# Performance work log

Measured on AMD Instinct MI355X. Metric: run time of the kernel, lower is better.

Reference implementation:

```python
import jax, jax.numpy as jnp
import numpy as np

NUM_HEADS = 16

def _rmsnorm(x, w):
    eps = jnp.finfo(x.dtype).eps  # torch nn.RMSNorm default eps
    ms = jnp.mean(x * x, axis=-1, keepdims=True)
    return x * jax.lax.rsqrt(ms + eps) * w

def _heads(x):
    B, S, D = x.shape
    return x.reshape(B, S, NUM_HEADS, D // NUM_HEADS)

def _attn(q, k, v):
    # q:[B,Sq,H,D] k,v:[B,Sk,H,D]; non-causal softmax attention
    scale = 1.0 / np.sqrt(q.shape[-1]).astype(np.float32)
    s = jnp.einsum('bqhd,bkhd->bhqk', q, k) * scale
    p = jax.nn.softmax(s, axis=-1)
    return jnp.einsum('bhqk,bkhd->bqhd', p, v)

def _gate(ctx, W1, b1, W2, b2):
    # Linear -> SiLU -> Linear(dim->1) -> sigmoid ; returns [B,S,1]
    h = jax.nn.silu(ctx @ W1.T + b1)
    return jax.nn.sigmoid(h @ W2.T + b2)

def setup_inputs() -> dict:
    key = jax.random.key(0)
    ks = jax.random.split(key, 20)
    B, Sq, Sk, St, dim = 4, 512, 2048, 512, 1024
    n = lambda k, shp, s=1.0: jax.random.normal(k, shp, jnp.float32) * s
    W = lambda k, o, i: n(k, (o, i), 0.02)
    return {
        'queries': n(ks[0], (B, Sq, dim)),
        'context_visual': n(ks[1], (B, Sk, dim)),
        'context_text': n(ks[2], (B, St, dim)),
        'w_norm_q': jnp.ones((dim,), jnp.float32),
        'w_norm_v': jnp.ones((dim,), jnp.float32),
        'w_norm_t': jnp.ones((dim,), jnp.float32),
        'Wq': W(ks[3], dim, dim), 'bq': n(ks[4], (dim,), 0.02),
        'Wk_vis': W(ks[5], dim, dim), 'bk_vis': jnp.zeros((dim,), jnp.float32),
        'Wv_vis': W(ks[6], dim, dim), 'bv_vis': jnp.zeros((dim,), jnp.float32),
        'Wk_text': W(ks[7], dim, dim), 'bk_text': jnp.zeros((dim,), jnp.float32),
        'Wv_text': W(ks[8], dim, dim), 'bv_text': jnp.zeros((dim,), jnp.float32),
        'Wg1v': W(ks[9], dim, dim), 'bg1v': jnp.zeros((dim,), jnp.float32),
        'Wg2v': W(ks[10], 1, dim), 'bg2v': jnp.zeros((1,), jnp.float32),
        'Wg1t': W(ks[11], dim, dim), 'bg1t': jnp.zeros((dim,), jnp.float32),
        'Wg2t': W(ks[12], 1, dim), 'bg2t': jnp.zeros((1,), jnp.float32),
        'Wo': W(ks[13], dim, dim), 'bo': jnp.zeros((dim,), jnp.float32),
    }

def reference(queries, context_visual, context_text,
              w_norm_q, w_norm_v, w_norm_t,
              Wq, bq, Wk_vis, bk_vis, Wv_vis, bv_vis,
              Wk_text, bk_text, Wv_text, bv_text,
              Wg1v, bg1v, Wg2v, bg2v, Wg1t, bg1t, Wg2t, bg2t,
              Wo, bo):
    residual = queries
    qn = _rmsnorm(queries, w_norm_q)
    cv = _rmsnorm(context_visual, w_norm_v)
    ct = _rmsnorm(context_text, w_norm_t)
    q = _heads(qn @ Wq.T + bq)
    k_vis = _heads(cv @ Wk_vis.T + bk_vis)
    v_vis = _heads(cv @ Wv_vis.T + bv_vis)
    v_vis = v_vis * _gate(cv, Wg1v, bg1v, Wg2v, bg2v)[..., None]  # [B,Sk,1,1]
    h = _attn(q, k_vis, v_vis)
    k_text = _heads(ct @ Wk_text.T + bk_text)
    v_text = _heads(ct @ Wv_text.T + bv_text)
    v_text = v_text * _gate(ct, Wg1t, bg1t, Wg2t, bg2t)[..., None]
    h = h + _attn(q, k_text, v_text)
    B, Sq, H, D = h.shape
    out = h.reshape(B, Sq, H * D) @ Wo.T + bo  # dropout p=0 -> identity
    return residual + out
```

## Files before the change

kernel.cpp:

```cpp
#include <hip/hip_runtime.h>
#include <hip/hip_bf16.h>

typedef __attribute__((ext_vector_type(4))) float f32x4;
typedef __attribute__((ext_vector_type(8))) short s16x8;
typedef __attribute__((ext_vector_type(4))) short s16x4;
using bf16 = __hip_bfloat16;

static constexpr int BB  = 4;
static constexpr int SQ  = 512;
static constexpr int SKV = 2048;
static constexpr int SKT = 512;
static constexpr int DIM = 1024;
static constexpr int NH  = 16;
static constexpr int HD  = 64;

#define MFMA32(A,B,C) __builtin_amdgcn_mfma_f32_16x16x32_bf16(A,B,C,0,0,0)

#if __has_builtin(__builtin_amdgcn_mfma_f32_16x16x16_bf16)
  #define MFMA16(A,B,C) __builtin_amdgcn_mfma_f32_16x16x16_bf16(A,B,C,0,0,0)
#elif __has_builtin(__builtin_amdgcn_mfma_f32_16x16x16bf16_1k)
  #define MFMA16(A,B,C) __builtin_amdgcn_mfma_f32_16x16x16bf16_1k(A,B,C,0,0,0)
#else
  #define MFMA16(A,B,C) (C)
#endif

#define SBAR() asm volatile("s_barrier" ::: "memory")

__device__ __forceinline__ float b2f(short s) {
  unsigned int u = ((unsigned int)(unsigned short)s) << 16;
  float f; __builtin_memcpy(&f, &u, 4); return f;
}
__device__ __forceinline__ short f2s(float f) {
  bf16 h = __float2bfloat16(f); short s; __builtin_memcpy(&s, &h, 2); return s;
}

__device__ __forceinline__ void gload16(const void* g, void* l) {
  __builtin_amdgcn_global_load_lds(
      (const __attribute__((address_space(1))) void*)g,
      (__attribute__((address_space(3))) void*)l, 16, 0, 0);
}

static constexpr float QSCALE = 0.180336880111120426f;

struct PrepArgs {
  const float* csrc[10]; bf16* cdst[10]; int cn[10];
  const float* nx[3]; const float* nw[3]; bf16* ny[3];
};
__global__ __launch_bounds__(256) void prep_kernel(PrepArgs a) {
  const int bx = blockIdx.x;
  if (bx < 10240) {
    const int y = bx >> 10;
    const int i = ((bx & 1023) * 256 + threadIdx.x) * 4;
    if (i >= a.cn[y]) return;
    const float4 v = *(const float4*)(a.csrc[y] + i);
    bf16* d = a.cdst[y] + i;
    d[0] = __float2bfloat16(v.x); d[1] = __float2bfloat16(v.y);
    d[2] = __float2bfloat16(v.z); d[3] = __float2bfloat16(v.w);
    return;
  }
  const int j = bx - 10240;
  int t, row;
  if (j < 2048) { t = 0; row = j; }
  else if (j < 10240) { t = 1; row = j - 2048; }
  else { t = 2; row = j - 10240; }
  const float* x = a.nx[t] + (size_t)row * DIM;
  const float4 v = *(const float4*)(x + threadIdx.x * 4);
  float ss = v.x*v.x + v.y*v.y + v.z*v.z + v.w*v.w;
  #pragma unroll
  for (int m = 32; m >= 1; m >>= 1) ss += __shfl_xor(ss, m);
  __shared__ float red[4];
  if ((threadIdx.x & 63) == 0) red[threadIdx.x >> 6] = ss;
  __syncthreads();
  ss = red[0] + red[1] + red[2] + red[3];
  const float sc = rsqrtf(ss * (1.0f / DIM) + 1.1920928955078125e-07f);
  const float4 w = *(const float4*)(a.nw[t] + threadIdx.x * 4);
  bf16* y = a.ny[t] + (size_t)row * DIM + threadIdx.x * 4;
  y[0] = __float2bfloat16(v.x * sc * w.x);
  y[1] = __float2bfloat16(v.y * sc * w.y);
  y[2] = __float2bfloat16(v.z * sc * w.z);
  y[3] = __float2bfloat16(v.w * sc * w.w);
}

struct PSlot { const bf16* A; const bf16* W; const float* bias;
               bf16* Cb; int epi; int sksh; };
struct PArgs { PSlot s[7]; };

__global__ __launch_bounds__(512, 2) void proj256(PArgs a) {
  __shared__ char lds[131072];
  const int tid = threadIdx.x, lane = tid & 63, wave = tid >> 6;
  const int m16 = lane & 15, g16 = lane >> 4;
  const int wm = wave >> 2, wn = wave & 3;

  const int i = (blockIdx.x & 7) * 64 + (blockIdx.x >> 3);
  int slot, rem;
  if (i < 384) { slot = i >> 7; rem = i & 127; }
  else { const int j = i - 384; slot = 3 + (j >> 5); rem = j & 31; }
  const PSlot S = a.s[slot];
  const int bn = rem & 3, bm = rem >> 2;

  const bf16* Ab = S.A + (size_t)bm * 256 * DIM;
  const bf16* Wb = S.W + (size_t)bn * 256 * DIM;

  auto stageAh = [&](int k0, int buf, int h) {
    #pragma unroll
    for (int q = 0; q < 2; ++q) {
      const int idx = (h * 2 + q) * 512 + tid;
      const int row = idx >> 3, g = (idx & 7) ^ (row & 7);
      gload16(Ab + (size_t)row * DIM + k0 + g * 8,
              &lds[buf * 65536 + (h * 2 + q) * 8192 + wave * 1024]);
    }
  };
  auto stageBfull = [&](int k0, int buf) {
    #pragma unroll
    for (int q = 0; q < 4; ++q) {
      const int idx = q * 512 + tid;
      const int row = idx >> 3, g = (idx & 7) ^ (row & 7);
      gload16(Wb + (size_t)row * DIM + k0 + g * 8,
              &lds[buf * 65536 + 32768 + q * 8192 + wave * 1024]);
    }
  };

  f32x4 acc[8][4];
  #pragma unroll
  for (int x = 0; x < 8; ++x)
    #pragma unroll
    for (int y = 0; y < 4; ++y)
      #pragma unroll
      for (int r = 0; r < 4; ++r) acc[x][y][r] = 0.0f;

  stageAh(0, 0, 0); stageAh(0, 0, 1);
  stageBfull(0, 0);
  stageBfull(64, 1);
  asm volatile("s_waitcnt vmcnt(4)" ::: "memory");
  SBAR();

  constexpr int NT = DIM / 64;
  for (int t = 0; t < NT; ++t) {
    const int buf = t & 1;
    const char* A0 = &lds[buf * 65536];
    const char* B0 = A0 + 32768;
    s16x8 af[4], bfk[4];

    #pragma unroll
    for (int mi = 0; mi < 4; ++mi) {
      const int row = wm * 128 + mi * 16 + m16;
      af[mi] = *(const s16x8*)(A0 + row * 128 + ((g16 ^ (m16 & 7)) * 16));
    }
    #pragma unroll
    for (int ni = 0; ni < 4; ++ni) {
      const int row = wn * 64 + ni * 16 + m16;
      bfk[ni] = *(const s16x8*)(B0 + row * 128 + ((g16 ^ (m16 & 7)) * 16));
    }
    if (t + 1 < NT) stageAh((t + 1) * 64, buf ^ 1, 0);
    SBAR();
    __builtin_amdgcn_s_setprio(1);
    #pragma unroll
    for (int mi = 0; mi < 4; ++mi)
      #pragma unroll
      for (int ni = 0; ni < 4; ++ni)
        acc[mi][ni] = MFMA32(af[mi], bfk[ni], acc[mi][ni]);
    __builtin_amdgcn_s_setprio(0);
    SBAR();

    #pragma unroll
    for (int mi = 0; mi < 4; ++mi) {
      const int row = wm * 128 + 64 + mi * 16 + m16;
      af[mi] = *(const s16x8*)(A0 + row * 128 + ((g16 ^ (m16 & 7)) * 16));
    }
    if (t + 1 < NT) stageAh((t + 1) * 64, buf ^ 1, 1);
    SBAR();
    __builtin_amdgcn_s_setprio(1);
    #pragma unroll
    for (int mi = 0; mi < 4; ++mi)
      #pragma unroll
      for (int ni = 0; ni < 4; ++ni)
        acc[4 + mi][ni] = MFMA32(af[mi], bfk[ni], acc[4 + mi][ni]);
    __builtin_amdgcn_s_setprio(0);
    SBAR();

    #pragma unroll
    for (int mi = 0; mi < 4; ++mi) {
      const int row = wm * 128 + mi * 16 + m16;
      af[mi] = *(const s16x8*)(A0 + row * 128 + (((4 + g16) ^ (m16 & 7)) * 16));
    }
    #pragma unroll
    for (int ni = 0; ni < 4; ++ni) {
      const int row = wn * 64 + ni * 16 + m16;
      bfk[ni] = *(const s16x8*)(B0 + row * 128 + (((4 + g16) ^ (m16 & 7)) * 16));
    }
    SBAR();
    __builtin_amdgcn_s_setprio(1);
    #pragma unroll
    for (int mi = 0; mi < 4; ++mi)
      #pragma unroll
      for (int ni = 0; ni < 4; ++ni)
        acc[mi][ni] = MFMA32(af[mi], bfk[ni], acc[mi][ni]);
    __builtin_amdgcn_s_setprio(0);
    SBAR();

    #pragma unroll
    for (int mi = 0; mi < 4; ++mi) {
      const int row = wm * 128 + 64 + mi * 16 + m16;
      af[mi] = *(const s16x8*)(A0 + row * 128 + (((4 + g16) ^ (m16 & 7)) * 16));
    }
    if (t + 2 < NT) stageBfull((t + 2) * 64, buf);
    SBAR();
    __builtin_amdgcn_s_setprio(1);
    #pragma unroll
    for (int mi = 0; mi < 4; ++mi)
      #pragma unroll
      for (int ni = 0; ni < 4; ++ni)
        acc[4 + mi][ni] = MFMA32(af[mi], bfk[ni], acc[4 + mi][ni]);
    __builtin_amdgcn_s_setprio(0);
    if (t < NT - 2)       { asm volatile("s_waitcnt vmcnt(4)" ::: "memory"); }
    else if (t == NT - 2) { asm volatile("s_waitcnt vmcnt(0)" ::: "memory"); }
    SBAR();
  }

  const int r0 = bm * 256 + wm * 128, c0 = bn * 256 + wn * 64;
  if (S.epi >= 3) {
    const float sc = (S.epi == 3) ? QSCALE : 1.0f;
    const int msk = (1 << S.sksh) - 1;
    #pragma unroll
    for (int ng = 0; ng < 4; ++ng) {
      const int col = c0 + ng * 16 + m16;
      const int hh = col >> 6, d = col & 63;
      const float bv = S.bias[col];
      #pragma unroll
      for (int mg = 0; mg < 8; ++mg) {
        const int rowb = r0 + mg * 16 + g16 * 4;
        #pragma unroll
        for (int r = 0; r < 4; ++r) {
          const int m = rowb + r;
          const int bb2 = m >> S.sksh, tok = m & msk;
          S.Cb[(((size_t)(bb2 * NH + hh) << S.sksh) + tok) * HD + d] =
              __float2bfloat16((acc[mg][ng][r] + bv) * sc);
        }
      }
    }
  } else {
    #pragma unroll
    for (int ng = 0; ng < 4; ++ng) {
      const int col = c0 + ng * 16 + m16;
      const float bv = S.bias[col];
      #pragma unroll
      for (int mg = 0; mg < 8; ++mg) {
        const int rowb = r0 + mg * 16 + g16 * 4;
        #pragma unroll
        for (int r = 0; r < 4; ++r) {
          float v = acc[mg][ng][r] + bv;
          const size_t idx = (size_t)(rowb + r) * DIM + col;
          if (S.epi == 1) { v = v / (1.0f + __expf(-v)); S.Cb[idx] = __float2bfloat16(v); }
          else            { S.Cb[idx] = __float2bfloat16(v); }
        }
      }
    }
  }
}

struct GSlot { const bf16* A; const bf16* W; const float* bias;
               const float* resid; float* Cf; };
__global__ __launch_bounds__(256) void gemm_out(GSlot S) {
  constexpr int K = DIM;
  __shared__ alignas(16) char sA[4096];
  __shared__ alignas(16) char sB[8192];
  const int tid = threadIdx.x, lane = tid & 63, wave = tid >> 6;
  const int bm = blockIdx.x, bn = blockIdx.y;
  const int m16 = lane & 15, g16 = lane >> 4;

  f32x4 acc[4][2];
  #pragma unroll
  for (int i = 0; i < 4; ++i)
    #pragma unroll
    for (int j = 0; j < 2; ++j)
      #pragma unroll
      for (int r = 0; r < 4; ++r) acc[i][j][r] = 0.0f;

  const bf16* Ab = S.A + (size_t)bm * 64 * K;
  const bf16* Wb = S.W + (size_t)bn * 128 * K;

  for (int t = 0; t < K / 32; ++t) {
    const int k0 = t * 32;
    {
      const int row = tid >> 2, sg = (tid & 3) ^ (row & 3);
      gload16(Ab + (size_t)row * K + k0 + sg * 8, &sA[wave * 1024]);
    }
    #pragma unroll
    for (int p = 0; p < 2; ++p) {
      const int idx = p * 256 + tid;
      const int row = idx >> 2, sg = (idx & 3) ^ (row & 3);
      gload16(Wb + (size_t)row * K + k0 + sg * 8, &sB[p * 4096 + wave * 1024]);
    }
    __syncthreads();
    s16x8 af[4], bfr[2];
    #pragma unroll
    for (int mi = 0; mi < 4; ++mi) {
      const int row = mi * 16 + m16;
      af[mi] = *(const s16x8*)(&sA[row * 64 + (g16 ^ (m16 & 3)) * 16]);
    }
    #pragma unroll
    for (int ni = 0; ni < 2; ++ni) {
      const int row = wave * 32 + ni * 16 + m16;
      bfr[ni] = *(const s16x8*)(&sB[row * 64 + (g16 ^ (m16 & 3)) * 16]);
    }
    #pragma unroll
    for (int mi = 0; mi < 4; ++mi)
      #pragma unroll
      for (int ni = 0; ni < 2; ++ni)
        acc[mi][ni] = MFMA32(af[mi], bfr[ni], acc[mi][ni]);
    __syncthreads();
  }

  const int r0 = bm * 64, c0 = bn * 128 + wave * 32;
  #pragma unroll
  for (int ni = 0; ni < 2; ++ni) {
    const int col = c0 + ni * 16 + m16;
    const float bv = S.bias[col];
    #pragma unroll
    for (int mi = 0; mi < 4; ++mi) {
      const int rowb = r0 + mi * 16 + g16 * 4;
      #pragma unroll
      for (int r = 0; r < 4; ++r) {
        const size_t idx = (size_t)(rowb + r) * DIM + col;
        S.Cf[idx] = acc[mi][ni][r] + bv + S.resid[idx];
      }
    }
  }
}

__global__ __launch_bounds__(256) void gate2_kernel(
    const bf16* __restrict__ g1v, const bf16* __restrict__ w2v,
    const float* __restrict__ b2v, float* __restrict__ gv,
    const bf16* __restrict__ g1t, const bf16* __restrict__ w2t,
    const float* __restrict__ b2t, float* __restrict__ gt)
{
  const int lane = threadIdx.x & 63, wave = threadIdx.x >> 6;
  int row = blockIdx.x * 4 + wave;
  const bf16* x; const bf16* w2; const float* b2; float* gate;
  if (row < BB * SKV) { x = g1v + (size_t)row * DIM; w2 = w2v; b2 = b2v; gate = gv + row; }
  else { row -= BB * SKV; x = g1t + (size_t)row * DIM; w2 = w2t; b2 = b2t; gate = gt + row; }
  float sum = 0.0f;
  #pragma unroll
  for (int c = 0; c < 2; ++c) {
    const int i0 = c * 512 + lane * 8;
    const s16x8 xv = *(const s16x8*)(x + i0);
    const s16x8 wv = *(const s16x8*)(w2 + i0);
    #pragma unroll
    for (int j = 0; j < 8; ++j) sum += b2f(xv[j]) * b2f(wv[j]);
  }
  #pragma unroll
  for (int m = 32; m >= 1; m >>= 1) sum += __shfl_xor(sum, m);
  if (lane == 0) *gate = 1.0f / (1.0f + __expf(-(sum + b2[0])));
}

__global__ __launch_bounds__(256) void vtrans2_kernel(
    const bf16* __restrict__ Vv, const float* __restrict__ gv, bf16* __restrict__ VTv,
    const bf16* __restrict__ Vt, const float* __restrict__ gt, bf16* __restrict__ VTt)
{
  __shared__ alignas(16) short tile[64][72];
  int kt = blockIdx.x;
  const bf16* V; const float* gate; bf16* VT; int Sk;
  if (kt < SKV / 64) { V = Vv; gate = gv; VT = VTv; Sk = SKV; }
  else { kt -= SKV / 64; V = Vt; gate = gt; VT = VTt; Sk = SKT; }
  const int h = blockIdx.y, b = blockIdx.z;
  const int tid = threadIdx.x;
  #pragma unroll
  for (int i = 0; i < 2; ++i) {
    const int c = tid + i * 256;
    const int kr = c >> 3, d0 = (c & 7) * 8;
    const float g = gate[(size_t)b * Sk + kt * 64 + kr];
    const s16x8 v = *(const s16x8*)(V + ((size_t)(b*Sk + kt*64 + kr)*NH + h)*HD + d0);
    #pragma unroll
    for (int j = 0; j < 8; ++j) tile[kr][d0 + j] = f2s(b2f(v[j]) * g);
  }
  __syncthreads();
  #pragma unroll
  for (int i = 0; i < 2; ++i) {
    const int c = tid + i * 256;
    const int d = c >> 3, k0 = (c & 7) * 8;
    s16x8 v;
    #pragma unroll
    for (int j = 0; j < 8; ++j) v[j] = tile[k0 + j][d];
    *(s16x8*)(VT + ((size_t)(b*NH + h)*HD + d)*Sk + kt*64 + k0) = v;
  }
}

__global__ __launch_bounds__(512, 2) void attn_kernel(
    const bf16* __restrict__ Qh,
    const bf16* __restrict__ K1h, const bf16* __restrict__ VT1,
    const bf16* __restrict__ K2h, const bf16* __restrict__ VT2,
    bf16* __restrict__ Hout)
{
  __shared__ alignas(16) char sK[2][2][8192];
  __shared__ alignas(16) char sVT[2][2][8192];
  const int tid = threadIdx.x, lane = tid & 63, wave = tid >> 6;
  const int hb = blockIdx.x;
  const int h = hb & 15, b = hb >> 4;
  const int wq = wave & 3, hf = wave >> 2;
  const int q0 = blockIdx.y * 64 + wq * 16;
  const int m16 = lane & 15, g16 = lane >> 4;

  const bf16* qrow = Qh + ((size_t)(b*NH + h)*SQ + q0 + m16)*HD;
  const s16x8 qf0 = *(const s16x8*)(qrow + g16 * 8);
  const s16x8 qf1 = *(const s16x8*)(qrow + 32 + g16 * 8);

  const bf16* K1b  = K1h + (size_t)(b*NH + h) * SKV * HD;
  const bf16* K2b  = K2h + (size_t)(b*NH + h) * SKT * HD;
  const bf16* VT1b = VT1 + (size_t)(b*NH + h) * HD * SKV;
  const bf16* VT2b = VT2 + (size_t)(b*NH + h) * HD * SKT;

  constexpr int NC1 = SKV / 128, NC = NC1 + SKT / 128;

  auto stage = [&](int c, int buf) {
    const int ctx = (c >= NC1);
    const bf16* Kb  = ctx ? K2b  : K1b;
    const bf16* VTb = ctx ? VT2b : VT1b;
    const int Sk = ctx ? SKT : SKV;
    const int cc = ctx ? c - NC1 : c;
    const int b0 = cc * 64, b1 = (Sk >> 1) + cc * 64;
    const int r = tid >> 3, g = (tid & 7) ^ (r & 7);
    gload16(Kb  + (size_t)(b0 + r) * HD + g * 8, &sK[buf][0][wave * 1024]);
    gload16(Kb  + (size_t)(b1 + r) * HD + g * 8, &sK[buf][1][wave * 1024]);
    gload16(VTb + (size_t)r * Sk + b0 + g * 8,   &sVT[buf][0][wave * 1024]);
    gload16(VTb + (size_t)r * Sk + b1 + g * 8,   &sVT[buf][1][wave * 1024]);
  };

  f32x4 o[4], ov[4];
  float mx, l, mxv, lv;
  #pragma unroll
  for (int i = 0; i < 4; ++i)
    #pragma unroll
    for (int r = 0; r < 4; ++r) { o[i][r] = 0.0f; ov[i][r] = 0.0f; }
  mx = -1e30f; l = 0.0f; mxv = -1e30f; lv = 0.0f;

  auto chunk = [&](int buf) {
    const char* kbase = &sK[buf][hf][0];
    const char* vbase = &sVT[buf][hf][0];
    f32x4 s[4];
    #pragma unroll
    for (int nt = 0; nt < 4; ++nt) {
      const char* kr = kbase + (nt * 16 + m16) * 128;
      const s16x8 kf0 = *(const s16x8*)(kr + ((g16    ) ^ (m16 & 7)) * 16);
      const s16x8 kf1 = *(const s16x8*)(kr + ((4 + g16) ^ (m16 & 7)) * 16);
      f32x4 a2; a2[0] = 0; a2[1] = 0; a2[2] = 0; a2[3] = 0;
      a2 = MFMA32(kf0, qf0, a2);
      a2 = MFMA32(kf1, qf1, a2);
      s[nt] = a2;
    }
    float mc = s[0][0];
    #pragma unroll
    for (int nt = 0; nt < 4; ++nt)
      #pragma unroll
      for (int r = 0; r < 4; ++r) mc = fmaxf(mc, s[nt][r]);
    mc = fmaxf(mc, __shfl_xor(mc, 16));
    mc = fmaxf(mc, __shfl_xor(mc, 32));
    const float mnew = fmaxf(mx, mc);
    const float alpha = exp2f(mx - mnew);
    mx = mnew;
    float p[4][4]; float rs = 0.0f;
    #pragma unroll
    for (int nt = 0; nt < 4; ++nt)
      #pragma unroll
      for (int r = 0; r < 4; ++r) { p[nt][r] = exp2f(s[nt][r] - mnew); rs += p[nt][r]; }
    rs += __shfl_xor(rs, 16);
    rs += __shfl_xor(rs, 32);
    l = l * alpha + rs;
    float av[4];
    #pragma unroll
    for (int r = 0; r < 4; ++r) av[r] = __shfl(alpha, g16 * 4 + r);
    #pragma unroll
    for (int nd = 0; nd < 4; ++nd)
      #pragma unroll
      for (int r = 0; r < 4; ++r) o[nd][r] *= av[r];
    #pragma unroll
    for (int nt = 0; nt < 4; ++nt) {
      s16x4 pa;
      pa[0] = f2s(p[nt][0]); pa[1] = f2s(p[nt][1]);
      pa[2] = f2s(p[nt][2]); pa[3] = f2s(p[nt][3]);
      #pragma unroll
      for (int nd = 0; nd < 4; ++nd) {
        const int d = nd * 16 + m16;
        const int g = (nt * 2 + (g16 >> 1)) ^ (m16 & 7);
        const s16x4 vf = *(const s16x4*)(vbase + d * 128 + g * 16 + (g16 & 1) * 8);
        o[nd] = MFMA16(pa, vf, o[nd]);
      }
    }
  };

  stage(0, 0);
  asm volatile("s_waitcnt vmcnt(0)" ::: "memory");
  SBAR();

  int buf = 0;
  for (int c = 0; c < NC; ++c) {
    if (c + 1 < NC) stage(c + 1, buf ^ 1);
    chunk(buf);
    if (c == NC1 - 1) {
      #pragma unroll
      for (int nd = 0; nd < 4; ++nd) ov[nd] = o[nd];
      mxv = mx; lv = l;
      #pragma unroll
      for (int nd = 0; nd < 4; ++nd)
        #pragma unroll
        for (int r = 0; r < 4; ++r) o[nd][r] = 0.0f;
      mx = -1e30f; l = 0.0f;
    }
    asm volatile("s_waitcnt vmcnt(0)" ::: "memory");
    SBAR();
    buf ^= 1;
  }

  float* mo = (float*)&sK[0][0][0];
  float* ml = (float*)&sVT[0][0][0];
  if (hf) {
    #pragma unroll
    for (int nd = 0; nd < 4; ++nd)
      #pragma unroll
      for (int r = 0; r < 4; ++r) {
        const int rl = wq * 16 + g16 * 4 + r;
        mo[rl * 64 + nd * 16 + m16]        = ov[nd][r];
        mo[4096 + rl * 64 + nd * 16 + m16] = o[nd][r];
      }
    if (g16 == 0) {
      ml[(wq * 4 + 0) * 16 + m16] = mxv; ml[(wq * 4 + 1) * 16 + m16] = lv;
      ml[(wq * 4 + 2) * 16 + m16] = mx;  ml[(wq * 4 + 3) * 16 + m16] = l;
    }
  }
  __syncthreads();
  if (!hf) {
    float of[4][4];
    #pragma unroll
    for (int ctx = 0; ctx < 2; ++ctx) {
      const float mb = ml[(wq * 4 + ctx * 2 + 0) * 16 + m16];
      const float lb = ml[(wq * 4 + ctx * 2 + 1) * 16 + m16];
      const float ma = ctx ? mx : mxv;
      const float la = ctx ? l  : lv;
      const float ms = fmaxf(ma, mb);
      const float aA = exp2f(ma - ms), aB = exp2f(mb - ms);
      const float lt = la * aA + lb * aB;
      float aAv[4], aBv[4], ltv[4];
      #pragma unroll
      for (int r = 0; r < 4; ++r) {
        aAv[r] = __shfl(aA, g16 * 4 + r);
        aBv[r] = __shfl(aB, g16 * 4 + r);
        ltv[r] = __shfl(lt, g16 * 4 + r);
      }
      #pragma unroll
      for (int nd = 0; nd < 4; ++nd)
        #pragma unroll
        for (int r = 0; r < 4; ++r) {
          const int rl = wq * 16 + g16 * 4 + r;
          const float ob = mo[ctx * 4096 + rl * 64 + nd * 16 + m16];
          const float oa = ctx ? o[nd][r] : ov[nd][r];
          const float res = (oa * aAv[r] + ob * aBv[r]) / ltv[r];
          if (ctx == 0) of[nd][r] = res; else of[nd][r] += res;
        }
    }
    #pragma unroll
    for (int nd = 0; nd < 4; ++nd)
      #pragma unroll
      for (int r = 0; r < 4; ++r) {
        const int row = q0 + g16 * 4 + r;
        Hout[((size_t)(b*SQ + row)*NH + h)*HD + nd*16 + m16] =
            __float2bfloat16(of[nd][r]);
      }
  }
}

extern "C" void kernel_launch(void* const* d_in, const int* in_sizes, int n_in,
                              void* d_out, int out_size, void* d_ws, size_t ws_size,
                              hipStream_t stream)
{
  const float* queries = (const float*)d_in[0];
  const float* ctx_v   = (const float*)d_in[1];
  const float* ctx_t   = (const float*)d_in[2];
  const float* w_nq = (const float*)d_in[3];
  const float* w_nv = (const float*)d_in[4];
  const float* w_nt = (const float*)d_in[5];
  const float* Wq   = (const float*)d_in[6];  const float* bq   = (const float*)d_in[7];
  const float* Wk_v = (const float*)d_in[8];  const float* bk_v = (const float*)d_in[9];
  const float* Wv_v = (const float*)d_in[10]; const float* bv_v = (const float*)d_in[11];
  const float* Wk_t = (const float*)d_in[12]; const float* bk_t = (const float*)d_in[13];
  const float* Wv_t = (const float*)d_in[14]; const float* bv_t = (const float*)d_in[15];
  const float* Wg1v = (const float*)d_in[16]; const float* bg1v = (const float*)d_in[17];
  const float* Wg2v = (const float*)d_in[18]; const float* bg2v = (const float*)d_in[19];
  const float* Wg1t = (const float*)d_in[20]; const float* bg1t = (const float*)d_in[21];
  const float* Wg2t = (const float*)d_in[22]; const float* bg2t = (const float*)d_in[23];
  const float* Wo   = (const float*)d_in[24]; const float* bo   = (const float*)d_in[25];

  char* ws = (char*)d_ws;
  size_t off = 0;
  auto alloc = [&](size_t n) { void* p = ws + off; off += (n + 255) & ~(size_t)255; return p; };

  const size_t MATB = (size_t)DIM * DIM * 2;
  bf16* WqB   = (bf16*)alloc(MATB);
  bf16* WkvB  = (bf16*)alloc(MATB);
  bf16* WvvB  = (bf16*)alloc(MATB);
  bf16* WktB  = (bf16*)alloc(MATB);
  bf16* WvtB  = (bf16*)alloc(MATB);
  bf16* Wg1vB = (bf16*)alloc(MATB);
  bf16* Wg1tB = (bf16*)alloc(MATB);
  bf16* WoB   = (bf16*)alloc(MATB);
  bf16* Wg2vB = (bf16*)alloc(2048);
  bf16* Wg2tB = (bf16*)alloc(2048);

  bf16* qn  = (bf16*)alloc((size_t)BB*SQ*DIM*2);
  bf16* cv  = (bf16*)alloc((size_t)BB*SKV*DIM*2);
  bf16* ct  = (bf16*)alloc((size_t)BB*SKT*DIM*2);
  bf16* qb  = (bf16*)alloc((size_t)BB*SQ*DIM*2);
  bf16* kvB = (bf16*)alloc((size_t)BB*SKV*DIM*2);
  bf16* ktB = (bf16*)alloc((size_t)BB*SKT*DIM*2);
  bf16* vtV = (bf16*)alloc((size_t)BB*SKV*DIM*2);
  bf16* vtT = (bf16*)alloc((size_t)BB*SKT*DIM*2);
  bf16* vScrV = (bf16*)alloc((size_t)BB*SKV*DIM*2);
  bf16* vScrT = (bf16*)alloc((size_t)BB*SKT*DIM*2);
  bf16* g1V   = (bf16*)alloc((size_t)BB*SKV*DIM*2);
  bf16* g1T   = (bf16*)alloc((size_t)BB*SKT*DIM*2);
  float* gateV = (float*)alloc((size_t)BB*SKV*4);
  float* gateT = (float*)alloc((size_t)BB*SKT*4);
  bf16* hB  = (bf16*)alloc((size_t)BB*SQ*DIM*2);
  (void)ws_size; (void)n_in; (void)in_sizes; (void)out_size;

  PrepArgs pr;
  const float* wsrc[10] = {Wq, Wk_v, Wv_v, Wk_t, Wv_t, Wg1v, Wg1t, Wo, Wg2v, Wg2t};
  bf16* wdst[10] = {WqB, WkvB, WvvB, WktB, WvtB, Wg1vB, Wg1tB, WoB, Wg2vB, Wg2tB};
  for (int i = 0; i < 10; ++i) {
    pr.csrc[i] = wsrc[i]; pr.cdst[i] = wdst[i];
    pr.cn[i] = (i < 8) ? DIM * DIM : DIM;
  }
  pr.nx[0] = queries; pr.nx[1] = ctx_v; pr.nx[2] = ctx_t;
  pr.nw[0] = w_nq;    pr.nw[1] = w_nv;  pr.nw[2] = w_nt;
  pr.ny[0] = qn;      pr.ny[1] = cv;    pr.ny[2] = ct;
  prep_kernel<<<dim3(10240 + 12288), 256, 0, stream>>>(pr);

  PArgs pa;
  pa.s[0] = {cv, WkvB,  bk_v, kvB,   4, 11};
  pa.s[1] = {cv, WvvB,  bv_v, vScrV, 0, 0};
  pa.s[2] = {cv, Wg1vB, bg1v, g1V,   1, 0};
  pa.s[3] = {qn, WqB,   bq,   qb,    3, 9};
  pa.s[4] = {ct, WktB,  bk_t, ktB,   4, 9};
  pa.s[5] = {ct, WvtB,  bv_t, vScrT, 0, 0};
  pa.s[6] = {ct, Wg1tB, bg1t, g1T,   1, 0};
  proj256<<<dim3(512), 512, 0, stream>>>(pa);

  gate2_kernel<<<dim3((BB*SKV + BB*SKT) / 4), 256, 0, stream>>>(
      g1V, Wg2vB, bg2v, gateV, g1T, Wg2tB, bg2t, gateT);
  vtrans2_kernel<<<dim3(SKV/64 + SKT/64, NH, BB), 256, 0, stream>>>(
      vScrV, gateV, vtV, vScrT, gateT, vtT);

  attn_kernel<<<dim3(NH*BB, SQ/64), 512, 0, stream>>>(qb, kvB, vtV, ktB, vtT, hB);

  GSlot go{hB, WoB, bo, queries, (float*)d_out};
  gemm_out<<<dim3(BB*SQ/64, 8), 256, 0, stream>>>(go);
}
```

Baseline: 195.8 us.

## Give each attention wave its own query rows and triple-buffer K/V chunks

The attention kernel stops splitting the key range across two wave halves. All 8 waves now handle distinct 16-row query tiles, 128 queries per block, and share each 64-key K/VT chunk. This removes the cross-wave LDS merge of partial softmax states and doubles reuse of each staged K/V tile. Loads move to a 3-stage ring with a prefetch distance of two. The grid is halved to 256 blocks, which may hurt occupancy across the CUs, and there are twice as many loop iterations per block.

```diff
diff --git a/kernel.cpp b/kernel.cpp
--- a/kernel.cpp
+++ b/kernel.cpp
@@ -391,13 +391,12 @@
     const bf16* __restrict__ K2h, const bf16* __restrict__ VT2,
     bf16* __restrict__ Hout)
 {
-  __shared__ alignas(16) char sK[2][2][8192];
-  __shared__ alignas(16) char sVT[2][2][8192];
+  __shared__ alignas(16) char sK[3][8192];
+  __shared__ alignas(16) char sVT[3][8192];
   const int tid = threadIdx.x, lane = tid & 63, wave = tid >> 6;
   const int hb = blockIdx.x;
   const int h = hb & 15, b = hb >> 4;
-  const int wq = wave & 3, hf = wave >> 2;
-  const int q0 = blockIdx.y * 64 + wq * 16;
+  const int q0 = blockIdx.y * 128 + wave * 16;
   const int m16 = lane & 15, g16 = lane >> 4;
 
   const bf16* qrow = Qh + ((size_t)(b*NH + h)*SQ + q0 + m16)*HD;
@@ -409,33 +408,49 @@
   const bf16* VT1b = VT1 + (size_t)(b*NH + h) * HD * SKV;
   const bf16* VT2b = VT2 + (size_t)(b*NH + h) * HD * SKT;
 
-  constexpr int NC1 = SKV / 128, NC = NC1 + SKT / 128;
+  constexpr int NCV = SKV / 64, NC = NCV + SKT / 64;
 
   auto stage = [&](int c, int buf) {
-    const int ctx = (c >= NC1);
+    const int ctx = (c >= NCV);
     const bf16* Kb  = ctx ? K2b  : K1b;
     const bf16* VTb = ctx ? VT2b : VT1b;
     const int Sk = ctx ? SKT : SKV;
-    const int cc = ctx ? c - NC1 : c;
-    const int b0 = cc * 64, b1 = (Sk >> 1) + cc * 64;
+    const int b0 = (ctx ? c - NCV : c) * 64;
     const int r = tid >> 3, g = (tid & 7) ^ (r & 7);
-    gload16(Kb  + (size_t)(b0 + r) * HD + g * 8, &sK[buf][0][wave * 1024]);
-    gload16(Kb  + (size_t)(b1 + r) * HD + g * 8, &sK[buf][1][wave * 1024]);
-    gload16(VTb + (size_t)r * Sk + b0 + g * 8,   &sVT[buf][0][wave * 1024]);
-    gload16(VTb + (size_t)r * Sk + b1 + g * 8,   &sVT[buf][1][wave * 1024]);
+    gload16(Kb  + (size_t)(b0 + r) * HD + g * 8, &sK[buf][wave * 1024]);
+    gload16(VTb + (size_t)r * Sk + b0 + g * 8,   &sVT[buf][wave * 1024]);
   };
 
-  f32x4 o[4], ov[4];
-  float mx, l, mxv, lv;
+  float of[4][4];
   #pragma unroll
   for (int i = 0; i < 4; ++i)
     #pragma unroll
-    for (int r = 0; r < 4; ++r) { o[i][r] = 0.0f; ov[i][r] = 0.0f; }
-  mx = -1e30f; l = 0.0f; mxv = -1e30f; lv = 0.0f;
+    for (int r = 0; r < 4; ++r) of[i][r] = 0.0f;
+
+  f32x4 o[4];
+  float mx = -1e30f, l = 0.0f;
+  #pragma unroll
+  for (int i = 0; i < 4; ++i)
+    #pragma unroll
+    for (int r = 0; r < 4; ++r) o[i][r] = 0.0f;
+
+  auto flush = [&]() {
+    float lb[4];
+    #pragma unroll
+    for (int r = 0; r < 4; ++r) lb[r] = __shfl(l, g16 * 4 + r);
+    #pragma unroll
+    for (int nd = 0; nd < 4; ++nd)
+      #pragma unroll
+      for (int r = 0; r < 4; ++r) {
+        of[nd][r] += o[nd][r] / lb[r];
+        o[nd][r] = 0.0f;
+      }
+    mx = -1e30f; l = 0.0f;
+  };
 
   auto chunk = [&](int buf) {
-    const char* kbase = &sK[buf][hf][0];
-    const char* vbase = &sVT[buf][hf][0];
+    const char* kbase = &sK[buf][0];
+    const char* vbase = &sVT[buf][0];
     f32x4 s[4];
     #pragma unroll
     for (int nt = 0; nt < 4; ++nt) {
@@ -488,83 +503,28 @@
   };
 
   stage(0, 0);
-  asm volatile("s_waitcnt vmcnt(0)" ::: "memory");
+  stage(1, 1);
+  asm volatile("s_waitcnt vmcnt(2)" ::: "memory");
   SBAR();
 
-  int buf = 0;
   for (int c = 0; c < NC; ++c) {
-    if (c + 1 < NC) stage(c + 1, buf ^ 1);
-    chunk(buf);
-    if (c == NC1 - 1) {
-      #pragma unroll
-      for (int nd = 0; nd < 4; ++nd) ov[nd] = o[nd];
-      mxv = mx; lv = l;
-      #pragma unroll
-      for (int nd = 0; nd < 4; ++nd)
-        #pragma unroll
-        for (int r = 0; r < 4; ++r) o[nd][r] = 0.0f;
-      mx = -1e30f; l = 0.0f;
-    }
-    asm volatile("s_waitcnt vmcnt(0)" ::: "memory");
-    SBAR();
-    buf ^= 1;
-  }
-
-  float* mo = (float*)&sK[0][0][0];
-  float* ml = (float*)&sVT[0][0][0];
-  if (hf) {
-    #pragma unroll
-    for (int nd = 0; nd < 4; ++nd)
-      #pragma unroll
-      for (int r = 0; r < 4; ++r) {
-        const int rl = wq * 16 + g16 * 4 + r;
-        mo[rl * 64 + nd * 16 + m16]        = ov[nd][r];
-        mo[4096 + rl * 64 + nd * 16 + m16] = o[nd][r];
-      }
-    if (g16 == 0) {
-      ml[(wq * 4 + 0) * 16 + m16] = mxv; ml[(wq * 4 + 1) * 16 + m16] = lv;
-      ml[(wq * 4 + 2) * 16 + m16] = mx;  ml[(wq * 4 + 3) * 16 + m16] = l;
-    }
-  }
-  __syncthreads();
-  if (!hf) {
-    float of[4][4];
-    #pragma unroll
-    for (int ctx = 0; ctx < 2; ++ctx) {
-      const float mb = ml[(wq * 4 + ctx * 2 + 0) * 16 + m16];
-      const float lb = ml[(wq * 4 + ctx * 2 + 1) * 16 + m16];
-      const float ma = ctx ? mx : mxv;
-      const float la = ctx ? l  : lv;
-      const float ms = fmaxf(ma, mb);
-      const float aA = exp2f(ma - ms), aB = exp2f(mb - ms);
-      const float lt = la * aA + lb * aB;
-      float aAv[4], aBv[4], ltv[4];
-      #pragma unroll
-      for (int r = 0; r < 4; ++r) {
-        aAv[r] = __shfl(aA, g16 * 4 + r);
-        aBv[r] = __shfl(aB, g16 * 4 + r);
-        ltv[r] = __shfl(lt, g16 * 4 + r);
-      }
-      #pragma unroll
-      for (int nd = 0; nd < 4; ++nd)
-        #pragma unroll
-        for (int r = 0; r < 4; ++r) {
-          const int rl = wq * 16 + g16 * 4 + r;
-          const float ob = mo[ctx * 4096 + rl * 64 + nd * 16 + m16];
-          const float oa = ctx ? o[nd][r] : ov[nd][r];
-          const float res = (oa * aAv[r] + ob * aBv[r]) / ltv[r];
-          if (ctx == 0) of[nd][r] = res; else of[nd][r] += res;
-        }
-    }
-    #pragma unroll
-    for (int nd = 0; nd < 4; ++nd)
-      #pragma unroll
-      for (int r = 0; r < 4; ++r) {
-        const int row = q0 + g16 * 4 + r;
-        Hout[((size_t)(b*SQ + row)*NH + h)*HD + nd*16 + m16] =
-            __float2bfloat16(of[nd][r]);
-      }
-  }
+    if (c + 2 < NC) stage(c + 2, (c + 2) % 3);
+    chunk(c % 3);
+    if (c == NCV - 1) flush();
+    if (c + 2 < NC) { asm volatile("s_waitcnt vmcnt(2)" ::: "memory"); }
+    else            { asm volatile("s_waitcnt vmcnt(0)" ::: "memory"); }
+    SBAR();
+  }
+  flush();
+
+  #pragma unroll
+  for (int nd = 0; nd < 4; ++nd)
+    #pragma unroll
+    for (int r = 0; r < 4; ++r) {
+      const int row = q0 + g16 * 4 + r;
+      Hout[((size_t)(b*SQ + row)*NH + h)*HD + nd*16 + m16] =
+          __float2bfloat16(of[nd][r]);
+    }
 }
 
 extern "C" void kernel_launch(void* const* d_in, const int* in_sizes, int n_in,
@@ -648,7 +608,7 @@
   vtrans2_kernel<<<dim3(SKV/64 + SKT/64, NH, BB), 256, 0, stream>>>(
       vScrV, gateV, vtV, vScrT, gateT, vtT);
 
-  attn_kernel<<<dim3(NH*BB, SQ/64), 512, 0, stream>>>(qb, kvB, vtV, ktB, vtT, hB);
+  attn_kernel<<<dim3(NH*BB, SQ/128), 512, 0, stream>>>(qb, kvB, vtV, ktB, vtT, hB);
 
   GSlot go{hB, WoB, bo, queries, (float*)d_out};
   gemm_out<<<dim3(BB*SQ/64, 8), 256, 0, stream>>>(go);
```

New measurement: 217.1 us. +10.9%, slower.

## Replace double-buffered projection GEMM pipeline with single-buffered load-wait-compute loop

Applied to the files above, without the earlier changes.

The projection GEMM kernel drops its two-stage LDS double buffer and interleaved prefetch schedule. It now loads each 64-wide K tile into a single 64KB buffer, waits for all loads, then runs the MFMAs. Launch bounds are raised to 4 blocks per CU to hide memory latency through occupancy instead of software pipelining. The cost is that global loads no longer overlap compute within a block, and 512 threads at 4 blocks per CU with 128 accumulator floats per thread may force register spills.

```diff
diff --git a/kernel.cpp b/kernel.cpp
--- a/kernel.cpp
+++ b/kernel.cpp
@@ -85,8 +85,8 @@
                bf16* Cb; int epi; int sksh; };
 struct PArgs { PSlot s[7]; };
 
-__global__ __launch_bounds__(512, 2) void proj256(PArgs a) {
-  __shared__ char lds[131072];
+__global__ __launch_bounds__(512, 4) void proj256(PArgs a) {
+  __shared__ char lds[65536];
   const int tid = threadIdx.x, lane = tid & 63, wave = tid >> 6;
   const int m16 = lane & 15, g16 = lane >> 4;
   const int wm = wave >> 2, wn = wave & 3;
@@ -101,22 +101,22 @@
   const bf16* Ab = S.A + (size_t)bm * 256 * DIM;
   const bf16* Wb = S.W + (size_t)bn * 256 * DIM;
 
-  auto stageAh = [&](int k0, int buf, int h) {
-    #pragma unroll
-    for (int q = 0; q < 2; ++q) {
-      const int idx = (h * 2 + q) * 512 + tid;
+  auto stageA = [&](int k0) {
+    #pragma unroll
+    for (int q = 0; q < 4; ++q) {
+      const int idx = q * 512 + tid;
       const int row = idx >> 3, g = (idx & 7) ^ (row & 7);
       gload16(Ab + (size_t)row * DIM + k0 + g * 8,
-              &lds[buf * 65536 + (h * 2 + q) * 8192 + wave * 1024]);
+              &lds[q * 8192 + wave * 1024]);
     }
   };
-  auto stageBfull = [&](int k0, int buf) {
+  auto stageB = [&](int k0) {
     #pragma unroll
     for (int q = 0; q < 4; ++q) {
       const int idx = q * 512 + tid;
       const int row = idx >> 3, g = (idx & 7) ^ (row & 7);
       gload16(Wb + (size_t)row * DIM + k0 + g * 8,
-              &lds[buf * 65536 + 32768 + q * 8192 + wave * 1024]);
+              &lds[32768 + q * 8192 + wave * 1024]);
     }
   };
 
@@ -127,93 +127,43 @@
     for (int y = 0; y < 4; ++y)
       #pragma unroll
       for (int r = 0; r < 4; ++r) acc[x][y][r] = 0.0f;
-
-  stageAh(0, 0, 0); stageAh(0, 0, 1);
-  stageBfull(0, 0);
-  stageBfull(64, 1);
-  asm volatile("s_waitcnt vmcnt(4)" ::: "memory");
-  SBAR();
 
   constexpr int NT = DIM / 64;
   for (int t = 0; t < NT; ++t) {
-    const int buf = t & 1;
-    const char* A0 = &lds[buf * 65536];
-    const char* B0 = A0 + 32768;
-    s16x8 af[4], bfk[4];
-
-    #pragma unroll
-    for (int mi = 0; mi < 4; ++mi) {
-      const int row = wm * 128 + mi * 16 + m16;
-      af[mi] = *(const s16x8*)(A0 + row * 128 + ((g16 ^ (m16 & 7)) * 16));
-    }
+    const int k0 = t * 64;
+    stageA(k0); stageB(k0);
+    asm volatile("s_waitcnt vmcnt(0)" ::: "memory");
+    SBAR();
+    const char* A0 = &lds[0];
+    const char* B0 = &lds[32768];
+    s16x8 bfk[4][2];
     #pragma unroll
     for (int ni = 0; ni < 4; ++ni) {
       const int row = wn * 64 + ni * 16 + m16;
-      bfk[ni] = *(const s16x8*)(B0 + row * 128 + ((g16 ^ (m16 & 7)) * 16));
-    }
-    if (t + 1 < NT) stageAh((t + 1) * 64, buf ^ 1, 0);
-    SBAR();
-    __builtin_amdgcn_s_setprio(1);
-    #pragma unroll
-    for (int mi = 0; mi < 4; ++mi)
-      #pragma unroll
-      for (int ni = 0; ni < 4; ++ni)
-        acc[mi][ni] = MFMA32(af[mi], bfk[ni], acc[mi][ni]);
-    __builtin_amdgcn_s_setprio(0);
-    SBAR();
-
-    #pragma unroll
-    for (int mi = 0; mi < 4; ++mi) {
-      const int row = wm * 128 + 64 + mi * 16 + m16;
-      af[mi] = *(const s16x8*)(A0 + row * 128 + ((g16 ^ (m16 & 7)) * 16));
-    }
-    if (t + 1 < NT) stageAh((t + 1) * 64, buf ^ 1, 1);
-    SBAR();
-    __builtin_amdgcn_s_setprio(1);
-    #pragma unroll
-    for (int mi = 0; mi < 4; ++mi)
-      #pragma unroll
-      for (int ni = 0; ni < 4; ++ni)
-        acc[4 + mi][ni] = MFMA32(af[mi], bfk[ni], acc[4 + mi][ni]);
-    __builtin_amdgcn_s_setprio(0);
-    SBAR();
-
-    #pragma unroll
-    for (int mi = 0; mi < 4; ++mi) {
-      const int row = wm * 128 + mi * 16 + m16;
-      af[mi] = *(const s16x8*)(A0 + row * 128 + (((4 + g16) ^ (m16 & 7)) * 16));
-    }
-    #pragma unroll
-    for (int ni = 0; ni < 4; ++ni) {
-      const int row = wn * 64 + ni * 16 + m16;
-      bfk[ni] = *(const s16x8*)(B0 + row * 128 + (((4 + g16) ^ (m16 & 7)) * 16));
-    }
-    SBAR();
-    __builtin_amdgcn_s_setprio(1);
-    #pragma unroll
-    for (int mi = 0; mi < 4; ++mi)
-      #pragma unroll
-      for (int ni = 0; ni < 4; ++ni)
-        acc[mi][ni] = MFMA32(af[mi], bfk[ni], acc[mi][ni]);
-    __builtin_amdgcn_s_setprio(0);
-    SBAR();
-
-    #pragma unroll
-    for (int mi = 0; mi < 4; ++mi) {
-      const int row = wm * 128 + 64 + mi * 16 + m16;
-      af[mi] = *(const s16x8*)(A0 + row * 128 + (((4 + g16) ^ (m16 & 7)) * 16));
-    }
-    if (t + 2 < NT) stageBfull((t + 2) * 64, buf);
-    SBAR();
-    __builtin_amdgcn_s_setprio(1);
-    #pragma unroll
-    for (int mi = 0; mi < 4; ++mi)
-      #pragma unroll
-      for (int ni = 0; ni < 4; ++ni)
-        acc[4 + mi][ni] = MFMA32(af[mi], bfk[ni], acc[4 + mi][ni]);
-    __builtin_amdgcn_s_setprio(0);
-    if (t < NT - 2)       { asm volatile("s_waitcnt vmcnt(4)" ::: "memory"); }
-    else if (t == NT - 2) { asm volatile("s_waitcnt vmcnt(0)" ::: "memory"); }
+      #pragma unroll
+      for (int ks = 0; ks < 2; ++ks)
+        bfk[ni][ks] = *(const s16x8*)(B0 + row * 128 + (((ks*4+g16) ^ (m16 & 7)) * 16));
+    }
+    #pragma unroll
+    for (int mh = 0; mh < 2; ++mh) {
+      s16x8 af[4][2];
+      #pragma unroll
+      for (int mi = 0; mi < 4; ++mi) {
+        const int row = wm * 128 + mh * 64 + mi * 16 + m16;
+        #pragma unroll
+        for (int ks = 0; ks < 2; ++ks)
+          af[mi][ks] = *(const s16x8*)(A0 + row * 128 + (((ks*4+g16) ^ (m16 & 7)) * 16));
+      }
+      __builtin_amdgcn_s_setprio(1);
+      #pragma unroll
+      for (int mi = 0; mi < 4; ++mi)
+        #pragma unroll
+        for (int ni = 0; ni < 4; ++ni) {
+          acc[mh*4+mi][ni] = MFMA32(af[mi][0], bfk[ni][0], acc[mh*4+mi][ni]);
+          acc[mh*4+mi][ni] = MFMA32(af[mi][1], bfk[ni][1], acc[mh*4+mi][ni]);
+        }
+      __builtin_amdgcn_s_setprio(0);
+    }
     SBAR();
   }
 
```

Measured after the change: 680.7 us. 248% more time.
